# Kernel tuning notes

Measured on AMD Instinct MI355X. Metric: run time of the kernel, lower is better.

The kernel has to match this reference:

```python
import jax, jax.numpy as jnp
import numpy as np
from jax import lax


def _max_pool(x, w):
    # x: (B, C, D, H, W); w: 3-tuple spatial window; stride 1, SAME via k//2 pad.
    window = (1, 1) + w
    pads = [(0, 0), (0, 0)] + [(k // 2, k // 2) for k in w]
    return lax.reduce_window(x, -jnp.inf, lax.max, window, (1,) * 5, pads)


def _min_pool(x, w):
    # torch max_pool pads with -inf, so min_pool = -max_pool(-x) exactly.
    return -_max_pool(-x, w)


def soft_skeletonize(x, thresh_width=5):
    for _ in range(thresh_width):
        p1 = _min_pool(x, (3, 1, 1))
        p2 = _min_pool(x, (1, 3, 1))
        p3 = _min_pool(x, (1, 1, 3))
        min_pool_x = jnp.minimum(jnp.minimum(p1, p2), p3)
        contour = jax.nn.relu(_max_pool(min_pool_x, (3, 3, 3)) - min_pool_x)
        x = jax.nn.relu(x - contour)
    return x


def positive_intersection(center_line, vessel):
    clf = center_line.reshape(center_line.shape[0], center_line.shape[1], -1)
    vf = vessel.reshape(vessel.shape[0], vessel.shape[1], -1)
    intersection = (clf * vf).sum(-1)          # (B, C)
    return (intersection.sum(0) + 1e-12) / (clf.sum(-1).sum(0) + 1e-12)  # (C,)


def setup_inputs() -> dict:
    key = jax.random.key(0)
    k1, k2 = jax.random.split(key)
    shape = (2, 1, 192, 192, 192)
    pred = jax.random.uniform(k1, shape, dtype=jnp.float32)
    target = jax.random.uniform(k2, shape, dtype=jnp.float32)
    return {"pred": pred, "target": target}


def reference(pred, target):
    target_skeleton = soft_skeletonize(target)
    cl_pred = soft_skeletonize(pred)
    clrecall = positive_intersection(target_skeleton, pred)[0]
    clacc = positive_intersection(cl_pred, target)[0]
    cldice = 2.0 * clrecall * clacc / (clrecall + clacc)
    return 1.0 - cldice
```

## Files before the change

kernel.cpp:

```cpp
#include <hip/hip_runtime.h>
#include <cfloat>


constexpr int D = 192, H = 192, W = 192, B = 2;
constexpr int HW = H * W;
constexpr int VOL = D * HW;
constexpr int CZ = 24;
constexpr int NCH = D / CZ;
constexpr int WPB = 4;
constexpr int NGY = H / WPB;
constexpr int STEPS = 30;
constexpr int NPART = B * NCH * H;

struct F3 { float x, y, z; };

__device__ __forceinline__ float min3f(float a, float b, float c) {
  return fminf(fminf(a, b), c);
}
__device__ __forceinline__ float max3f(float a, float b, float c) {
  return fmaxf(fmaxf(a, b), c);
}

__global__ __launch_bounds__(256, 4) void skel_iter(
    const float* __restrict__ srcA, float* __restrict__ dstA,
    const float* __restrict__ othA, double* __restrict__ partA,
    const float* __restrict__ srcB, float* __restrict__ dstB,
    const float* __restrict__ othB, double* __restrict__ partB,
    int last) {
  const int tid = threadIdx.x;
  const int lane = tid & 63;
  const int wv = tid >> 6;

  const int nwg = gridDim.x * gridDim.y * gridDim.z;
  int wid = blockIdx.x + gridDim.x * (blockIdx.y + gridDim.y * blockIdx.z);
  wid = (wid & 7) * (nwg >> 3) + (wid >> 3);
  const int gyg = wid % NGY;
  const int combo = wid / NGY;
  const int chunk = combo % NCH;
  const int bz = combo / NCH;
  const int b = bz % B;
  const int chain = bz / B;

  const int gy = gyg * WPB + wv;

  const float* __restrict__ vs = (chain ? srcB : srcA) + (size_t)b * VOL;
  float* __restrict__ vd = (chain ? dstB : dstA) + (size_t)b * VOL;
  const float* __restrict__ vo = (chain ? othB : othA) + (size_t)b * VOL;
  double* __restrict__ part = chain ? partB : partA;

  const int z0 = chunk * CZ;
  const int c0 = 3 * lane;

  int rb[5];
  #pragma unroll
  for (int r = 0; r < 5; ++r) rb[r] = min(max(gy - 2 + r, 0), H - 1) * W + c0;
  const bool ytop = (gy == 0), ybot = (gy == H - 1);
  const bool l0 = (lane == 0), l63 = (lane == 63);

  float xa[5][5][3];
  float Mprev[3];
  float h1[3], h2[3];
  float sp = 0.0f, ss = 0.0f;

  {
    const float* ps = vs + (size_t)max(z0 - 2, 0) * HW;
    #pragma unroll
    for (int r = 0; r < 5; ++r) {
      const F3 v = *(const F3*)(ps + rb[r]);
      xa[3][r][0] = v.x; xa[3][r][1] = v.y; xa[3][r][2] = v.z;
    }
    ps = vs + (size_t)max(z0 - 1, 0) * HW;
    #pragma unroll
    for (int r = 0; r < 5; ++r) {
      const F3 v = *(const F3*)(ps + rb[r]);
      xa[4][r][0] = v.x; xa[4][r][1] = v.y; xa[4][r][2] = v.z;
    }
    ps = vs + (size_t)z0 * HW;
    #pragma unroll
    for (int r = 0; r < 5; ++r) {
      const F3 v = *(const F3*)(ps + rb[r]);
      xa[0][r][0] = v.x; xa[0][r][1] = v.y; xa[0][r][2] = v.z;
    }
  }

  #pragma unroll 1
  for (int s5 = 0; s5 < STEPS; s5 += 5) {
    #pragma unroll
    for (int p = 0; p < 5; ++p) {
      const int s = s5 + p;
      const int z = z0 - 1 + s;
      const int LD  = (p + 1) % 5;
      const int SM2 = (p + 2) % 5;
      const int SM1 = (p + 3) % 5;
      const int SC  = (p + 4) % 5;

      {
        const int zc = min(z + 2, D - 1);
        const float* ps = vs + (size_t)zc * HW;
        #pragma unroll
        for (int r = 0; r < 5; ++r) {
          const F3 v = *(const F3*)(ps + rb[r]);
          xa[LD][r][0] = v.x; xa[LD][r][1] = v.y; xa[LD][r][2] = v.z;
        }
      }
      const int zo = z - 2;
      const bool emit = (s >= 3) && (s <= CZ + 2);
      float w0 = 0.f, w1 = 0.f, w2 = 0.f;
      if (last && emit) {
        const F3 wv3 = *(const F3*)(vo + (size_t)zo * HW + rb[2]);
        w0 = wv3.x; w1 = wv3.y; w2 = wv3.z;
      }

      float xl[3], xr[3];
      #pragma unroll
      for (int r = 0; r < 3; ++r) {
        xl[r] = __shfl_up(xa[SM1][r + 1][2], 1, 64);
        xr[r] = __shfl_down(xa[SM1][r + 1][0], 1, 64);
        if (l0) xl[r] = FLT_MAX;
        if (l63) xr[r] = FLT_MAX;
      }
      float Mc[3][3];
      #pragma unroll
      for (int r = 0; r < 3; ++r) {
        #pragma unroll
        for (int c = 0; c < 3; ++c) {
          const float le = (c == 0) ? xl[r] : xa[SM1][r + 1][c - 1];
          const float ri = (c == 2) ? xr[r] : xa[SM1][r + 1][c + 1];
          float v = min3f(xa[SM1][r + 1][c], le, ri);
          v = min3f(v, xa[SM1][r][c], xa[SM1][r + 2][c]);
          v = min3f(v, xa[SM2][r + 1][c], xa[SC][r + 1][c]);
          Mc[r][c] = v;
        }
      }
      if (ytop) { Mc[0][0] = Mc[0][1] = Mc[0][2] = -FLT_MAX; }
      if (ybot) { Mc[2][0] = Mc[2][1] = Mc[2][2] = -FLT_MAX; }

      float rm[3];
      #pragma unroll
      for (int c = 0; c < 3; ++c) rm[c] = max3f(Mc[0][c], Mc[1][c], Mc[2][c]);
      float ml = __shfl_up(rm[2], 1, 64);
      float mr = __shfl_down(rm[0], 1, 64);
      if (l0) ml = -FLT_MAX;
      if (l63) mr = -FLT_MAX;
      float h0c[3];
      h0c[0] = max3f(ml, rm[0], rm[1]);
      h0c[1] = max3f(rm[0], rm[1], rm[2]);
      h0c[2] = max3f(rm[1], rm[2], mr);

      if (emit) {
        const bool zlo = (zo > 0), zhi = (zo < D - 1);
        float o[3];
        #pragma unroll
        for (int c = 0; c < 3; ++c) {
          float P = h1[c];
          if (zlo) P = fmaxf(P, h2[c]);
          if (zhi) P = fmaxf(P, h0c[c]);
          const float contour = fmaxf(P - Mprev[c], 0.0f);
          o[c] = fmaxf(xa[SM2][2][c] - contour, 0.0f);
        }
        if (last) {
          sp += o[0] * w0 + o[1] * w1 + o[2] * w2;
          ss += o[0] + o[1] + o[2];
        } else {
          *(F3*)(vd + (size_t)zo * HW + rb[2]) = {o[0], o[1], o[2]};
        }
      }

      #pragma unroll
      for (int c = 0; c < 3; ++c) {
        h2[c] = h1[c];
        h1[c] = h0c[c];
        Mprev[c] = Mc[1][c];
      }
    }
  }

  if (last) {
    #pragma unroll
    for (int off = 32; off > 0; off >>= 1) {
      sp += __shfl_down(sp, off, 64);
      ss += __shfl_down(ss, off, 64);
    }
    if (lane == 0) {
      const int lin = (b * NCH + chunk) * H + gy;
      part[2 * lin] = (double)sp;
      part[2 * lin + 1] = (double)ss;
    }
  }
}

__global__ void finalize_kernel(const double* __restrict__ pa,
                                const double* __restrict__ pb,
                                float* __restrict__ out, int npart) {
  __shared__ double red[4][4];
  double s[4] = {0, 0, 0, 0};
  for (int i = threadIdx.x; i < npart; i += 256) {
    s[0] += pa[2 * i];
    s[1] += pa[2 * i + 1];
    s[2] += pb[2 * i];
    s[3] += pb[2 * i + 1];
  }
  #pragma unroll
  for (int off = 32; off > 0; off >>= 1)
    #pragma unroll
    for (int j = 0; j < 4; ++j) s[j] += __shfl_down(s[j], off, 64);
  const int wave = threadIdx.x >> 6, lane = threadIdx.x & 63;
  if (lane == 0)
    for (int j = 0; j < 4; ++j) red[j][wave] = s[j];
  __syncthreads();
  if (threadIdx.x == 0) {
    double t[4];
    for (int j = 0; j < 4; ++j)
      t[j] = red[j][0] + red[j][1] + red[j][2] + red[j][3];
    const double recall = (t[0] + 1e-12) / (t[1] + 1e-12);
    const double accv = (t[2] + 1e-12) / (t[3] + 1e-12);
    const double cldice = 2.0 * recall * accv / (recall + accv);
    out[0] = (float)(1.0 - cldice);
  }
}

extern "C" void kernel_launch(void* const* d_in, const int* in_sizes, int n_in,
                              void* d_out, int out_size, void* d_ws, size_t ws_size,
                              hipStream_t stream) {
  const float* pred = (const float*)d_in[0];
  const float* target = (const float*)d_in[1];
  float* out = (float*)d_out;
  const size_t NT = (size_t)VOL * B;

  const dim3 blk(256, 1, 1);
  const size_t need_merged = 4 * NT * sizeof(float) + 4 * NPART * sizeof(double);

  if (ws_size >= need_merged) {
    float* a0 = (float*)d_ws;
    float* a1 = a0 + NT;
    float* c0 = a1 + NT;
    float* c1 = c0 + NT;
    double* pA = (double*)(c1 + NT);
    double* pB = pA + 2 * NPART;
    const dim3 grd(NGY, NCH, 2 * B);
    skel_iter<<<grd, blk, 0, stream>>>(target, a0, pred, pA, pred, c0, target, pB, 0);
    skel_iter<<<grd, blk, 0, stream>>>(a0, a1, pred, pA, c0, c1, target, pB, 0);
    skel_iter<<<grd, blk, 0, stream>>>(a1, a0, pred, pA, c1, c0, target, pB, 0);
    skel_iter<<<grd, blk, 0, stream>>>(a0, a1, pred, pA, c0, c1, target, pB, 0);
    skel_iter<<<grd, blk, 0, stream>>>(a1, a0, pred, pA, c1, c0, target, pB, 1);
    finalize_kernel<<<1, 256, 0, stream>>>(pA, pB, out, NPART);
  } else {
    float* b0 = (float*)d_ws;
    float* b1 = b0 + NT;
    double* pA = (double*)(b1 + NT);
    double* pB = pA + 2 * NPART;
    const dim3 grd(NGY, NCH, B);
    skel_iter<<<grd, blk, 0, stream>>>(target, b0, pred, pA, nullptr, nullptr, nullptr, nullptr, 0);
    skel_iter<<<grd, blk, 0, stream>>>(b0, b1, pred, pA, nullptr, nullptr, nullptr, nullptr, 0);
    skel_iter<<<grd, blk, 0, stream>>>(b1, b0, pred, pA, nullptr, nullptr, nullptr, nullptr, 0);
    skel_iter<<<grd, blk, 0, stream>>>(b0, b1, pred, pA, nullptr, nullptr, nullptr, nullptr, 0);
    skel_iter<<<grd, blk, 0, stream>>>(b1, b0, pred, pA, nullptr, nullptr, nullptr, nullptr, 1);
    skel_iter<<<grd, blk, 0, stream>>>(pred, b0, target, pB, nullptr, nullptr, nullptr, nullptr, 0);
    skel_iter<<<grd, blk, 0, stream>>>(b0, b1, target, pB, nullptr, nullptr, nullptr, nullptr, 0);
    skel_iter<<<grd, blk, 0, stream>>>(b1, b0, target, pB, nullptr, nullptr, nullptr, nullptr, 0);
    skel_iter<<<grd, blk, 0, stream>>>(b0, b1, target, pB, nullptr, nullptr, nullptr, nullptr, 0);
    skel_iter<<<grd, blk, 0, stream>>>(b1, b0, target, pB, nullptr, nullptr, nullptr, nullptr, 1);
    finalize_kernel<<<1, 256, 0, stream>>>(pA, pB, out, NPART);
  }
}
```

Baseline: 385.2 us.

## Stage z-planes into LDS via async global_load_lds with a 4-slot ring

Each workgroup now cooperatively loads the 8 y-rows of every z-plane it needs into a 4-slot LDS ring with direct global-to-LDS loads. Each wave then reads its 5-row stencil from LDS instead of issuing 5 redundant global loads per plane. Stores become unconditional, with non-emitting steps redirected to a per-workgroup dump buffer so the vmcnt-based waits stay uniform. The cost is extra barriers per step, two extra pipeline steps per chunk, dummy stores, and fragile hand-counted waitcnt values.

```diff
diff --git a/kernel.cpp b/kernel.cpp
--- a/kernel.cpp
+++ b/kernel.cpp
@@ -9,10 +9,14 @@
 constexpr int NCH = D / CZ;
 constexpr int WPB = 4;
 constexpr int NGY = H / WPB;
-constexpr int STEPS = 30;
+constexpr int STEPS = 32;
 constexpr int NPART = B * NCH * H;
+constexpr int MAXWG = NGY * NCH * 2 * B;
 
 struct F3 { float x, y, z; };
+
+typedef __attribute__((address_space(3))) float lds_f;
+typedef __attribute__((address_space(1))) const float glb_f;
 
 __device__ __forceinline__ float min3f(float a, float b, float c) {
   return fminf(fminf(a, b), c);
@@ -26,14 +30,13 @@
     const float* __restrict__ othA, double* __restrict__ partA,
     const float* __restrict__ srcB, float* __restrict__ dstB,
     const float* __restrict__ othB, double* __restrict__ partB,
-    int last) {
-  const int tid = threadIdx.x;
-  const int lane = tid & 63;
-  const int wv = tid >> 6;
-
+    float* __restrict__ dump, int last) {
+  __shared__ float slab[4][8][192];
+
+  const int tid = threadIdx.x, lane = tid & 63, wv = tid >> 6;
+  const int bid0 = blockIdx.x + gridDim.x * (blockIdx.y + gridDim.y * blockIdx.z);
   const int nwg = gridDim.x * gridDim.y * gridDim.z;
-  int wid = blockIdx.x + gridDim.x * (blockIdx.y + gridDim.y * blockIdx.z);
-  wid = (wid & 7) * (nwg >> 3) + (wid >> 3);
+  const int wid = (bid0 & 7) * (nwg >> 3) + (bid0 >> 3);
   const int gyg = wid % NGY;
   const int combo = wid / NGY;
   const int chunk = combo % NCH;
@@ -41,7 +44,8 @@
   const int b = bz % B;
   const int chain = bz / B;
 
-  const int gy = gyg * WPB + wv;
+  const int gy0 = gyg * WPB;
+  const int gy = gy0 + wv;
 
   const float* __restrict__ vs = (chain ? srcB : srcA) + (size_t)b * VOL;
   float* __restrict__ vd = (chain ? dstB : dstA) + (size_t)b * VOL;
@@ -50,72 +54,96 @@
 
   const int z0 = chunk * CZ;
   const int c0 = 3 * lane;
-
-  int rb[5];
+  const int wrow = gy * W + c0;
+  float* __restrict__ dmp = dump + (size_t)bid0 * 192 + c0;
+
+  int roff[5];
   #pragma unroll
-  for (int r = 0; r < 5; ++r) rb[r] = min(max(gy - 2 + r, 0), H - 1) * W + c0;
+  for (int r = 0; r < 5; ++r) {
+    const int i = min(max(gy - 2 + r, 0), H - 1) - (gy0 - 2);
+    roff[r] = i * 192 + c0;
+  }
   const bool ytop = (gy == 0), ybot = (gy == H - 1);
   const bool l0 = (lane == 0), l63 = (lane == 63);
 
-  float xa[5][5][3];
-  float Mprev[3];
-  float h1[3], h2[3];
+  const int g0 = min(max(gy0 - 2 + wv, 0), H - 1);
+  const int g1 = min(max(gy0 + 2 + wv, 0), H - 1);
+
+  auto stage = [&](int plane, int slot) {
+    const int zc = min(max(plane, 0), D - 1);
+    const float* s0 = vs + (size_t)zc * HW + (size_t)g0 * W + c0;
+    const float* s1 = vs + (size_t)zc * HW + (size_t)g1 * W + c0;
+    __builtin_amdgcn_global_load_lds((glb_f*)s0, (lds_f*)&slab[slot][wv][0], 12, 0, 0);
+    __builtin_amdgcn_global_load_lds((glb_f*)s1, (lds_f*)&slab[slot][wv + 4][0], 12, 0, 0);
+  };
+
+  float xa[4][5][3];
+  float Mprev[3] = {0, 0, 0}, h1[3] = {0, 0, 0}, h2[3] = {0, 0, 0};
   float sp = 0.0f, ss = 0.0f;
 
+  stage(z0 - 3, 0);
+  stage(z0 - 2, 1);
+  stage(z0 - 1, 2);
+  asm volatile("s_waitcnt vmcnt(0)" ::: "memory");
+  __builtin_amdgcn_s_barrier();
+  __builtin_amdgcn_sched_barrier(0);
   {
-    const float* ps = vs + (size_t)max(z0 - 2, 0) * HW;
+    const float* sp0 = &slab[0][0][0];
+    const float* sp1 = &slab[1][0][0];
+    #pragma unroll
+    for (int r = 1; r <= 3; ++r) {
+      xa[2][r][0] = sp0[roff[r]]; xa[2][r][1] = sp0[roff[r] + 1]; xa[2][r][2] = sp0[roff[r] + 2];
+    }
     #pragma unroll
     for (int r = 0; r < 5; ++r) {
-      const F3 v = *(const F3*)(ps + rb[r]);
-      xa[3][r][0] = v.x; xa[3][r][1] = v.y; xa[3][r][2] = v.z;
-    }
-    ps = vs + (size_t)max(z0 - 1, 0) * HW;
-    #pragma unroll
-    for (int r = 0; r < 5; ++r) {
-      const F3 v = *(const F3*)(ps + rb[r]);
-      xa[4][r][0] = v.x; xa[4][r][1] = v.y; xa[4][r][2] = v.z;
-    }
-    ps = vs + (size_t)z0 * HW;
-    #pragma unroll
-    for (int r = 0; r < 5; ++r) {
-      const F3 v = *(const F3*)(ps + rb[r]);
-      xa[0][r][0] = v.x; xa[0][r][1] = v.y; xa[0][r][2] = v.z;
-    }
-  }
+      xa[3][r][0] = sp1[roff[r]]; xa[3][r][1] = sp1[roff[r] + 1]; xa[3][r][2] = sp1[roff[r] + 2];
+    }
+  }
+  xa[2][0][0] = xa[2][0][1] = xa[2][0][2] = 0.0f;
+  xa[2][4][0] = xa[2][4][1] = xa[2][4][2] = 0.0f;
+  stage(z0, 3);
+  *(F3*)dmp = {0.0f, 0.0f, 0.0f};
+  asm volatile("s_waitcnt lgkmcnt(0)" ::: "memory");
+  __builtin_amdgcn_s_barrier();
+  __builtin_amdgcn_sched_barrier(0);
 
   #pragma unroll 1
-  for (int s5 = 0; s5 < STEPS; s5 += 5) {
-    #pragma unroll
-    for (int p = 0; p < 5; ++p) {
-      const int s = s5 + p;
+  for (int s4 = 0; s4 < STEPS; s4 += 4) {
+    #pragma unroll
+    for (int p = 0; p < 4; ++p) {
+      const int s = s4 + p;
       const int z = z0 - 1 + s;
-      const int LD  = (p + 1) % 5;
-      const int SM2 = (p + 2) % 5;
-      const int SM1 = (p + 3) % 5;
-      const int SC  = (p + 4) % 5;
+      const int zo = z - 2;
+      const bool emit = (s >= 3) && (s <= CZ + 2);
+      const int NEW = p, OLD = (p + 2) & 3, MID = (p + 3) & 3;
+      const int RS = (p + 2) & 3;
+
+      float w0 = 0.f, w1 = 0.f, w2 = 0.f;
+      if (last) {
+        const F3 wv3 = *(const F3*)(emit ? (vo + (size_t)zo * HW + wrow) : (vo + wrow));
+        w0 = wv3.x; w1 = wv3.y; w2 = wv3.z;
+      }
+      stage(z + 2, p);
+      if (last) asm volatile("s_waitcnt vmcnt(8)" ::: "memory");
+      else      asm volatile("s_waitcnt vmcnt(6)" ::: "memory");
+      __builtin_amdgcn_s_barrier();
+      __builtin_amdgcn_sched_barrier(0);
 
       {
-        const int zc = min(z + 2, D - 1);
-        const float* ps = vs + (size_t)zc * HW;
+        const float* rp = &slab[RS][0][0];
         #pragma unroll
         for (int r = 0; r < 5; ++r) {
-          const F3 v = *(const F3*)(ps + rb[r]);
-          xa[LD][r][0] = v.x; xa[LD][r][1] = v.y; xa[LD][r][2] = v.z;
-        }
-      }
-      const int zo = z - 2;
-      const bool emit = (s >= 3) && (s <= CZ + 2);
-      float w0 = 0.f, w1 = 0.f, w2 = 0.f;
-      if (last && emit) {
-        const F3 wv3 = *(const F3*)(vo + (size_t)zo * HW + rb[2]);
-        w0 = wv3.x; w1 = wv3.y; w2 = wv3.z;
+          xa[NEW][r][0] = rp[roff[r]];
+          xa[NEW][r][1] = rp[roff[r] + 1];
+          xa[NEW][r][2] = rp[roff[r] + 2];
+        }
       }
 
       float xl[3], xr[3];
       #pragma unroll
       for (int r = 0; r < 3; ++r) {
-        xl[r] = __shfl_up(xa[SM1][r + 1][2], 1, 64);
-        xr[r] = __shfl_down(xa[SM1][r + 1][0], 1, 64);
+        xl[r] = __shfl_up(xa[MID][r + 1][2], 1, 64);
+        xr[r] = __shfl_down(xa[MID][r + 1][0], 1, 64);
         if (l0) xl[r] = FLT_MAX;
         if (l63) xr[r] = FLT_MAX;
       }
@@ -124,11 +152,11 @@
       for (int r = 0; r < 3; ++r) {
         #pragma unroll
         for (int c = 0; c < 3; ++c) {
-          const float le = (c == 0) ? xl[r] : xa[SM1][r + 1][c - 1];
-          const float ri = (c == 2) ? xr[r] : xa[SM1][r + 1][c + 1];
-          float v = min3f(xa[SM1][r + 1][c], le, ri);
-          v = min3f(v, xa[SM1][r][c], xa[SM1][r + 2][c]);
-          v = min3f(v, xa[SM2][r + 1][c], xa[SC][r + 1][c]);
+          const float le = (c == 0) ? xl[r] : xa[MID][r + 1][c - 1];
+          const float ri = (c == 2) ? xr[r] : xa[MID][r + 1][c + 1];
+          float v = min3f(xa[MID][r + 1][c], le, ri);
+          v = min3f(v, xa[MID][r][c], xa[MID][r + 2][c]);
+          v = min3f(v, xa[OLD][r + 1][c], xa[NEW][r + 1][c]);
           Mc[r][c] = v;
         }
       }
@@ -147,7 +175,7 @@
       h0c[1] = max3f(rm[0], rm[1], rm[2]);
       h0c[2] = max3f(rm[1], rm[2], mr);
 
-      if (emit) {
+      {
         const bool zlo = (zo > 0), zhi = (zo < D - 1);
         float o[3];
         #pragma unroll
@@ -156,21 +184,18 @@
           if (zlo) P = fmaxf(P, h2[c]);
           if (zhi) P = fmaxf(P, h0c[c]);
           const float contour = fmaxf(P - Mprev[c], 0.0f);
-          o[c] = fmaxf(xa[SM2][2][c] - contour, 0.0f);
-        }
-        if (last) {
+          o[c] = fmaxf(xa[OLD][2][c] - contour, 0.0f);
+        }
+        float* dst = (!last && emit) ? (vd + (size_t)zo * HW + wrow) : dmp;
+        *(F3*)dst = {o[0], o[1], o[2]};
+        if (last && emit) {
           sp += o[0] * w0 + o[1] * w1 + o[2] * w2;
           ss += o[0] + o[1] + o[2];
-        } else {
-          *(F3*)(vd + (size_t)zo * HW + rb[2]) = {o[0], o[1], o[2]};
-        }
-      }
-
+        }
+      }
       #pragma unroll
       for (int c = 0; c < 3; ++c) {
-        h2[c] = h1[c];
-        h1[c] = h0c[c];
-        Mprev[c] = Mc[1][c];
+        h2[c] = h1[c]; h1[c] = h0c[c]; Mprev[c] = Mc[1][c];
       }
     }
   }
@@ -226,9 +251,11 @@
   const float* target = (const float*)d_in[1];
   float* out = (float*)d_out;
   const size_t NT = (size_t)VOL * B;
+  const size_t DUMPSZ = (size_t)MAXWG * 192;
 
   const dim3 blk(256, 1, 1);
-  const size_t need_merged = 4 * NT * sizeof(float) + 4 * NPART * sizeof(double);
+  const size_t need_merged =
+      4 * NT * sizeof(float) + 4 * NPART * sizeof(double) + DUMPSZ * sizeof(float);
 
   if (ws_size >= need_merged) {
     float* a0 = (float*)d_ws;
@@ -237,29 +264,31 @@
     float* c1 = c0 + NT;
     double* pA = (double*)(c1 + NT);
     double* pB = pA + 2 * NPART;
+    float* dump = (float*)(pB + 2 * NPART);
     const dim3 grd(NGY, NCH, 2 * B);
-    skel_iter<<<grd, blk, 0, stream>>>(target, a0, pred, pA, pred, c0, target, pB, 0);
-    skel_iter<<<grd, blk, 0, stream>>>(a0, a1, pred, pA, c0, c1, target, pB, 0);
-    skel_iter<<<grd, blk, 0, stream>>>(a1, a0, pred, pA, c1, c0, target, pB, 0);
-    skel_iter<<<grd, blk, 0, stream>>>(a0, a1, pred, pA, c0, c1, target, pB, 0);
-    skel_iter<<<grd, blk, 0, stream>>>(a1, a0, pred, pA, c1, c0, target, pB, 1);
+    skel_iter<<<grd, blk, 0, stream>>>(target, a0, pred, pA, pred, c0, target, pB, dump, 0);
+    skel_iter<<<grd, blk, 0, stream>>>(a0, a1, pred, pA, c0, c1, target, pB, dump, 0);
+    skel_iter<<<grd, blk, 0, stream>>>(a1, a0, pred, pA, c1, c0, target, pB, dump, 0);
+    skel_iter<<<grd, blk, 0, stream>>>(a0, a1, pred, pA, c0, c1, target, pB, dump, 0);
+    skel_iter<<<grd, blk, 0, stream>>>(a1, a0, pred, pA, c1, c0, target, pB, dump, 1);
     finalize_kernel<<<1, 256, 0, stream>>>(pA, pB, out, NPART);
   } else {
     float* b0 = (float*)d_ws;
     float* b1 = b0 + NT;
     double* pA = (double*)(b1 + NT);
     double* pB = pA + 2 * NPART;
+    float* dump = (float*)(pB + 2 * NPART);
     const dim3 grd(NGY, NCH, B);
-    skel_iter<<<grd, blk, 0, stream>>>(target, b0, pred, pA, nullptr, nullptr, nullptr, nullptr, 0);
-    skel_iter<<<grd, blk, 0, stream>>>(b0, b1, pred, pA, nullptr, nullptr, nullptr, nullptr, 0);
-    skel_iter<<<grd, blk, 0, stream>>>(b1, b0, pred, pA, nullptr, nullptr, nullptr, nullptr, 0);
-    skel_iter<<<grd, blk, 0, stream>>>(b0, b1, pred, pA, nullptr, nullptr, nullptr, nullptr, 0);
-    skel_iter<<<grd, blk, 0, stream>>>(b1, b0, pred, pA, nullptr, nullptr, nullptr, nullptr, 1);
-    skel_iter<<<grd, blk, 0, stream>>>(pred, b0, target, pB, nullptr, nullptr, nullptr, nullptr, 0);
-    skel_iter<<<grd, blk, 0, stream>>>(b0, b1, target, pB, nullptr, nullptr, nullptr, nullptr, 0);
-    skel_iter<<<grd, blk, 0, stream>>>(b1, b0, target, pB, nullptr, nullptr, nullptr, nullptr, 0);
-    skel_iter<<<grd, blk, 0, stream>>>(b0, b1, target, pB, nullptr, nullptr, nullptr, nullptr, 0);
-    skel_iter<<<grd, blk, 0, stream>>>(b1, b0, target, pB, nullptr, nullptr, nullptr, nullptr, 1);
+    skel_iter<<<grd, blk, 0, stream>>>(target, b0, pred, pA, nullptr, nullptr, nullptr, nullptr, dump, 0);
+    skel_iter<<<grd, blk, 0, stream>>>(b0, b1, pred, pA, nullptr, nullptr, nullptr, nullptr, dump, 0);
+    skel_iter<<<grd, blk, 0, stream>>>(b1, b0, pred, pA, nullptr, nullptr, nullptr, nullptr, dump, 0);
+    skel_iter<<<grd, blk, 0, stream>>>(b0, b1, pred, pA, nullptr, nullptr, nullptr, nullptr, dump, 0);
+    skel_iter<<<grd, blk, 0, stream>>>(b1, b0, pred, pA, nullptr, nullptr, nullptr, nullptr, dump, 1);
+    skel_iter<<<grd, blk, 0, stream>>>(pred, b0, target, pB, nullptr, nullptr, nullptr, nullptr, dump, 0);
+    skel_iter<<<grd, blk, 0, stream>>>(b0, b1, target, pB, nullptr, nullptr, nullptr, nullptr, dump, 0);
+    skel_iter<<<grd, blk, 0, stream>>>(b1, b0, target, pB, nullptr, nullptr, nullptr, nullptr, dump, 0);
+    skel_iter<<<grd, blk, 0, stream>>>(b0, b1, target, pB, nullptr, nullptr, nullptr, nullptr, dump, 0);
+    skel_iter<<<grd, blk, 0, stream>>>(b1, b0, target, pB, nullptr, nullptr, nullptr, nullptr, dump, 1);
     finalize_kernel<<<1, 256, 0, stream>>>(pA, pB, out, NPART);
   }
 }
```

After: 408.5 us. 6.1% more time.
